# Kernel tuning notes

Hardware: AMD Instinct MI355X
Metric: run time of the kernel (lower is better)

Reference implementation:

```python
import jax, jax.numpy as jnp
import numpy as np

NUM_HEADS = 8
OUT_FEATURES = 64
ALPHA = 0.2


def setup_inputs() -> dict:
    key = jax.random.key(0)
    k1, k2, k3, k4 = jax.random.split(key, 4)
    B, N, E, F_IN = 2, 8192, 4096, 256
    x = jax.random.normal(k1, (B, N, F_IN), dtype=jnp.float32)
    H = jax.random.uniform(k2, (N, E), dtype=jnp.float32)
    # xavier-like scaled params
    W = jax.random.normal(k3, (F_IN, OUT_FEATURES * NUM_HEADS), dtype=jnp.float32) * 0.05
    a_vertices = jax.random.normal(k4, (OUT_FEATURES, 1), dtype=jnp.float32) * 0.1
    return {"x": x, "H": H, "W": W, "a_vertices": a_vertices}


def reference(x, H, W, a_vertices):
    B, N, _ = x.shape
    # Wh: (B, N, heads, out)
    Wh = jnp.matmul(x, W).reshape(B, N, NUM_HEADS, OUT_FEATURES)
    # per-node, per-head attention logit: (B, N, heads)
    av = jax.nn.leaky_relu(jnp.einsum('bnhd,d->bnh', Wh, a_vertices[:, 0]), ALPHA)
    # edge attention: softmax over edges (torch dim=0 of (E, heads))
    ae = jax.nn.softmax(jnp.einsum('ne,bnh->beh', H, av), axis=1)  # (B, E, heads)
    # aggregate node features onto edges: (B, E, heads, out)
    m = jnp.einsum('ne,bnhd->behd', H, Wh)
    # scatter back to nodes with edge-attention weighting: (B, N, heads, out)
    out = jnp.einsum('ne,beh,behd->bnhd', H, ae, m)
    return out.reshape(B, N, NUM_HEADS * OUT_FEATURES)
```

## Files before the change

### kernel.cpp

```cpp
#include <hip/hip_runtime.h>

#define N_NODES 8192
#define N_EDGES 4096
#define F_INS   256
#define HEADS   8
#define DOUT    64
#define HDIM    512
#define CCOMB   1024
#define BATCH   2

typedef __bf16 bf16x8 __attribute__((ext_vector_type(8)));
typedef __bf16 bf16x4 __attribute__((ext_vector_type(4)));
typedef float  f32x4  __attribute__((ext_vector_type(4)));

__device__ __forceinline__ void gld_lds16(const __bf16* g, __bf16* l) {
    __builtin_amdgcn_global_load_lds(
        (const __attribute__((address_space(1))) void*)g,
        (__attribute__((address_space(3))) void*)l, 16, 0, 0);
}

__launch_bounds__(256)
__global__ void convert_H_logits_kernel(const float* __restrict__ H,
                                        const float* __restrict__ av,
                                        __bf16* __restrict__ Hb,
                                        __bf16* __restrict__ HbT,
                                        float* __restrict__ logits) {
    __shared__ float lav[512 * 16];
    __shared__ __bf16 tile[32][33];
    __shared__ float red[256 * 16];
    int t = threadIdx.x;
    int e0 = blockIdx.x * 32;
    int n0 = blockIdx.y * 512;
    for (int p = t; p < 8192; p += 256) {
        int b = p >> 12, rem = p & 4095, i = rem >> 3, h = rem & 7;
        lav[i * 16 + b * 8 + h] = av[(size_t)b * (N_NODES * 8) + (size_t)(n0 + i) * 8 + h];
    }
    __syncthreads();
    int c = t & 31, r0 = t >> 5;
    float acc[16];
#pragma unroll
    for (int q = 0; q < 16; ++q) acc[q] = 0.f;
    for (int sub = 0; sub < 16; ++sub) {
        int nb = n0 + sub * 32;
#pragma unroll
        for (int p = 0; p < 4; ++p) {
            int r = p * 8 + r0;
            float v = H[(size_t)(nb + r) * N_EDGES + e0 + c];
            __bf16 bv = (__bf16)v;
            Hb[(size_t)(nb + r) * N_EDGES + e0 + c] = bv;
            tile[r][c] = bv;
            const float* lr = &lav[(sub * 32 + r) * 16];
#pragma unroll
            for (int q = 0; q < 16; ++q) acc[q] += v * lr[q];
        }
        __syncthreads();
#pragma unroll
        for (int p = 0; p < 4; ++p) {
            int er = p * 8 + r0;
            HbT[(size_t)(e0 + er) * N_NODES + nb + c] = tile[c][er];
        }
        __syncthreads();
    }
#pragma unroll
    for (int q = 0; q < 16; ++q) red[t * 16 + q] = acc[q];
    __syncthreads();
    for (int o = t; o < 512; o += 256) {
        int e = o & 31, q = o >> 5;
        float s = 0.f;
#pragma unroll
        for (int r8 = 0; r8 < 8; ++r8) s += red[(r8 * 32 + e) * 16 + q];
        atomicAdd(&logits[(size_t)q * N_EDGES + e0 + e], s);
    }
}

__launch_bounds__(256)
__global__ void wbt_kernel(const float* __restrict__ W, __bf16* __restrict__ WbT) {
    int i = blockIdx.x * 256 + threadIdx.x;
    int c = i >> 8, f = i & 255;
    WbT[i] = (__bf16)W[(size_t)f * HDIM + c];
}

__launch_bounds__(256)
__global__ void wa_kernel(const float* __restrict__ W, const float* __restrict__ a,
                          float* __restrict__ Wa) {
    int i = blockIdx.x * 256 + threadIdx.x;
    if (i >= F_INS * HEADS) return;
    int f = i >> 3, h = i & 7;
    float s = 0.f;
#pragma unroll 8
    for (int d = 0; d < DOUT; ++d) s += W[(size_t)f * HDIM + h * DOUT + d] * a[d];
    Wa[i] = s;
}

__launch_bounds__(256)
__global__ void av_kernel(const float* __restrict__ x, const float* __restrict__ Wa,
                          float* __restrict__ av, __bf16* __restrict__ xb) {
    __shared__ float lx[32][257];
    __shared__ float lwa[F_INS * HEADS];
    int t = threadIdx.x;
    size_t row0 = (size_t)blockIdx.x * 32;
    for (int p = t; p < F_INS * HEADS; p += 256) lwa[p] = Wa[p];
#pragma unroll
    for (int p = 0; p < 32; ++p) {
        float v = x[(row0 + p) * F_INS + t];
        lx[p][t] = v;
        xb[(row0 + p) * F_INS + t] = (__bf16)v;
    }
    __syncthreads();
    int r = t >> 3, h = t & 7;
    float acc = 0.f;
#pragma unroll 8
    for (int f = 0; f < F_INS; ++f) acc += lx[r][f] * lwa[f * 8 + h];
    av[(row0 + r) * 8 + h] = acc > 0.f ? acc : 0.2f * acc;
}

__launch_bounds__(256)
__global__ void softmax_kernel(float* __restrict__ logits) {
    __shared__ float red[4];
    __shared__ float reds[4];
    int t = threadIdx.x;
    float* row = logits + (size_t)blockIdx.x * N_EDGES;
    float mx = -1e30f;
    for (int i = t; i < N_EDGES; i += 256) mx = fmaxf(mx, row[i]);
#pragma unroll
    for (int o = 32; o > 0; o >>= 1) mx = fmaxf(mx, __shfl_xor(mx, o, 64));
    if ((t & 63) == 0) red[t >> 6] = mx;
    __syncthreads();
    mx = fmaxf(fmaxf(red[0], red[1]), fmaxf(red[2], red[3]));
    float s = 0.f;
    for (int i = t; i < N_EDGES; i += 256) {
        float v = expf(row[i] - mx);
        row[i] = v;
        s += v;
    }
#pragma unroll
    for (int o = 32; o > 0; o >>= 1) s += __shfl_xor(s, o, 64);
    if ((t & 63) == 0) reds[t >> 6] = s;
    __syncthreads();
    float inv = 1.0f / (reds[0] + reds[1] + reds[2] + reds[3]);
    for (int i = t; i < N_EDGES; i += 256) row[i] *= inv;
}

template <int MODE>
__launch_bounds__(256, 4)
__global__ void gemm_bt(const __bf16* __restrict__ A, const __bf16* __restrict__ BT,
                        int lda, int ldbt, int K,
                        size_t a_bz, size_t bt_bz, size_t out_z,
                        __bf16* __restrict__ outB, int ldo,
                        float* __restrict__ outF) {
    __shared__ __bf16 AsF[8192];
    __shared__ __bf16 BsF[8192];
    int t = threadIdx.x;
    int bz = blockIdx.z;
    A  += (size_t)bz * a_bz;
    BT += (size_t)bz * bt_bz;
    if (MODE == 0) outB += (size_t)bz * out_z;
    if (MODE == 1) outF += (size_t)bz * out_z;
    size_t m0 = (size_t)blockIdx.y * 128;
    size_t n0 = (size_t)blockIdx.x * 128;

    int lane = t & 63, wv = t >> 6;
    int ln = lane & 15, lk = lane >> 4;

    const __bf16* pA[4]; const __bf16* pB[4];
    __bf16* lA[4]; __bf16* lB[4];
#pragma unroll
    for (int p = 0; p < 4; ++p) {
        int bid = wv * 4 + p;
        int mb = bid >> 1, kb = bid & 1;
        pA[p] = A + (m0 + mb * 16 + ln) * (size_t)lda + kb * 32 + lk * 8;
        pB[p] = BT + (n0 + mb * 16 + ln) * (size_t)ldbt + kb * 32 + lk * 8;
        lA[p] = &AsF[bid * 512];
        lB[p] = &BsF[bid * 512];
    }

    int wm16 = (wv & 1) * 4, wn16 = (wv >> 1) * 4;
    f32x4 acc[4][4] = {};

    for (int k0 = 0; k0 < K; k0 += 64) {
        __syncthreads();
#pragma unroll
        for (int p = 0; p < 4; ++p) gld_lds16(pA[p] + k0, lA[p]);
#pragma unroll
        for (int p = 0; p < 4; ++p) gld_lds16(pB[p] + k0, lB[p]);
        __syncthreads();
#pragma unroll
        for (int ksb = 0; ksb < 2; ++ksb) {
            bf16x8 af[4], bfr[4];
#pragma unroll
            for (int i = 0; i < 4; ++i)
                af[i] = *(const bf16x8*)&AsF[((wm16 + i) * 2 + ksb) * 512 + lane * 8];
#pragma unroll
            for (int j = 0; j < 4; ++j)
                bfr[j] = *(const bf16x8*)&BsF[((wn16 + j) * 2 + ksb) * 512 + lane * 8];
#pragma unroll
            for (int i = 0; i < 4; ++i)
#pragma unroll
                for (int j = 0; j < 4; ++j)
                    acc[i][j] = __builtin_amdgcn_mfma_f32_16x16x32_bf16(
                        af[i], bfr[j], acc[i][j], 0, 0, 0);
        }
    }

    int wm = (wv & 1) * 64, wn = (wv >> 1) * 64;
#pragma unroll
    for (int i = 0; i < 4; ++i)
#pragma unroll
        for (int j = 0; j < 4; ++j)
#pragma unroll
            for (int rg = 0; rg < 4; ++rg) {
                int gm = (int)m0 + wm + i * 16 + lk * 4 + rg;
                int gc = (int)n0 + wn + j * 16 + ln;
                float v = acc[i][j][rg];
                if (MODE == 0) {
                    outB[(size_t)gm * ldo + gc] = (__bf16)v;
                } else if (MODE == 1) {
                    outF[(size_t)gm * ldo + gc] = v;
                } else {
                    outF[(size_t)(gc >> 9) * ((size_t)N_NODES * HDIM) +
                         (size_t)gm * HDIM + (gc & 511)] = v;
                }
            }
}

template <int SWZ>
__launch_bounds__(512, 2)
__global__ void gemm256(const __bf16* __restrict__ A, const __bf16* __restrict__ BT,
                        int lda, int ldbt, int K,
                        size_t a_bz, size_t bt_bz, size_t out_z,
                        float* __restrict__ outF, int ldo) {
    __shared__ __bf16 lds[4 * 32 * 512];
    int bx, by, bz;
    if (SWZ) {
        int g = (int)blockIdx.x + 4 * ((int)blockIdx.y + 32 * (int)blockIdx.z);
        int xcd = g & 7, j = g >> 3;
        int l = (j & 3) + 4 * xcd + 32 * (j >> 2);
        bx = l & 3; by = (l >> 2) & 31; bz = l >> 7;
    } else {
        bx = blockIdx.x; by = blockIdx.y; bz = blockIdx.z;
    }
    A    += (size_t)bz * a_bz;
    BT   += (size_t)bz * bt_bz;
    outF += (size_t)bz * out_z;
    size_t m0 = (size_t)by * 256;
    size_t n0 = (size_t)bx * 256;

    int t = threadIdx.x;
    int lane = t & 63, wv = t >> 6;
    int ln = lane & 15, lk = lane >> 4;

    int fw = wv * 2;
    const __bf16* gA0 = A + (m0 + fw * 16 + ln) * (size_t)lda + lk * 8;
    const __bf16* gA1 = gA0 + 16 * (size_t)lda;
    const __bf16* gB0 = BT + (n0 + fw * 16 + ln) * (size_t)ldbt + lk * 8;
    const __bf16* gB1 = gB0 + 16 * (size_t)ldbt;

    int NT = K >> 5;

    for (int tt = 0; tt < 3; ++tt) {
        __bf16* d = &lds[tt * 16384];
        gld_lds16(gA0 + tt * 32, d + fw * 512);
        gld_lds16(gA1 + tt * 32, d + (fw + 1) * 512);
        gld_lds16(gB0 + tt * 32, d + (16 + fw) * 512);
        gld_lds16(gB1 + tt * 32, d + (16 + fw + 1) * 512);
    }
    asm volatile("s_waitcnt vmcnt(8)" ::: "memory");
    __builtin_amdgcn_s_barrier();
    __builtin_amdgcn_sched_barrier(0);

    f32x4 acc[8][4] = {};
    int wmf = (wv >> 2) * 8;
    int wnf = (wv & 3) * 4;

    auto compute = [&](int tl) {
        const __bf16* buf = &lds[(tl & 3) * 16384];
        bf16x8 af[8], bfr[4];
#pragma unroll
        for (int i = 0; i < 8; ++i)
            af[i] = *(const bf16x8*)(buf + (wmf + i) * 512 + lane * 8);
#pragma unroll
        for (int j = 0; j < 4; ++j)
            bfr[j] = *(const bf16x8*)(buf + (16 + wnf + j) * 512 + lane * 8);
        __builtin_amdgcn_s_setprio(1);
#pragma unroll
        for (int i = 0; i < 8; ++i)
#pragma unroll
            for (int j = 0; j < 4; ++j)
                acc[i][j] = __builtin_amdgcn_mfma_f32_16x16x32_bf16(
                    af[i], bfr[j], acc[i][j], 0, 0, 0);
        __builtin_amdgcn_s_setprio(0);
    };

    for (int tl = 0; tl < NT - 3; ++tl) {
        __bf16* d = &lds[((tl + 3) & 3) * 16384];
        int off = (tl + 3) * 32;
        gld_lds16(gA0 + off, d + fw * 512);
        gld_lds16(gA1 + off, d + (fw + 1) * 512);
        gld_lds16(gB0 + off, d + (16 + fw) * 512);
        gld_lds16(gB1 + off, d + (16 + fw + 1) * 512);
        compute(tl);
        asm volatile("s_waitcnt vmcnt(8)" ::: "memory");
        __builtin_amdgcn_s_barrier();
        __builtin_amdgcn_sched_barrier(0);
    }
    compute(NT - 3);
    asm volatile("s_waitcnt vmcnt(4)" ::: "memory");
    __builtin_amdgcn_s_barrier();
    __builtin_amdgcn_sched_barrier(0);
    compute(NT - 2);
    asm volatile("s_waitcnt vmcnt(0)" ::: "memory");
    __builtin_amdgcn_s_barrier();
    __builtin_amdgcn_sched_barrier(0);
    compute(NT - 1);

    int wm = (wv >> 2) * 128, wn = (wv & 3) * 64;
#pragma unroll
    for (int i = 0; i < 8; ++i)
#pragma unroll
        for (int j = 0; j < 4; ++j)
#pragma unroll
            for (int rg = 0; rg < 4; ++rg) {
                int gm = (int)m0 + wm + i * 16 + lk * 4 + rg;
                int gc = (int)n0 + wn + j * 16 + ln;
                outF[(size_t)gm * ldo + gc] = acc[i][j][rg];
            }
}

__launch_bounds__(256)
__global__ void scale1_kernel(const float* __restrict__ acc1, const float* __restrict__ ae,
                              __bf16* __restrict__ mwT) {
    int i = blockIdx.x * 256 + threadIdx.x;
    size_t base = (size_t)i * 4;
    int c = (int)(base >> 12);
    int e = (int)(base & 4095);
    const size_t slab = (size_t)CCOMB * N_EDGES / 4;
    float4 s0 = ((const float4*)acc1)[i];
    float4 s1 = ((const float4*)acc1)[i + slab];
    float4 s2 = ((const float4*)acc1)[i + 2 * slab];
    float4 s3 = ((const float4*)acc1)[i + 3 * slab];
    float4 a4 = *(const float4*)(ae + ((size_t)(c >> 6) << 12) + e);
    bf16x4 o;
    o.x = (__bf16)((s0.x + s1.x + s2.x + s3.x) * a4.x);
    o.y = (__bf16)((s0.y + s1.y + s2.y + s3.y) * a4.y);
    o.z = (__bf16)((s0.z + s1.z + s2.z + s3.z) * a4.z);
    o.w = (__bf16)((s0.w + s1.w + s2.w + s3.w) * a4.w);
    ((bf16x4*)mwT)[i] = o;
}

__launch_bounds__(256)
__global__ void reduce2_kernel(const float* __restrict__ s, float* __restrict__ out) {
    int i = blockIdx.x * 256 + threadIdx.x;
    size_t base = (size_t)i * 4;
    int m = (int)(base >> 10);
    int c = (int)(base & 1023);
    const size_t slab = (size_t)N_NODES * CCOMB / 4;
    float4 a = ((const float4*)s)[i];
    float4 b = ((const float4*)s)[i + slab];
    float4 o;
    o.x = a.x + b.x; o.y = a.y + b.y; o.z = a.z + b.z; o.w = a.w + b.w;
    *(float4*)&out[(size_t)(c >> 9) * ((size_t)N_NODES * HDIM) +
                   (size_t)m * HDIM + (c & 511)] = o;
}

extern "C" void kernel_launch(void* const* d_in, const int* in_sizes, int n_in,
                              void* d_out, int out_size, void* d_ws, size_t ws_size,
                              hipStream_t stream) {
    const float* x = (const float*)d_in[0];
    const float* H = (const float*)d_in[1];
    const float* W = (const float*)d_in[2];
    const float* a = (const float*)d_in[3];
    float* out = (float*)d_out;

    char* p = (char*)d_ws;
    __bf16* Hb   = (__bf16*)p; p += (size_t)N_NODES * N_EDGES * 2;
    __bf16* HbT  = (__bf16*)p; p += (size_t)N_EDGES * N_NODES * 2;
    __bf16* xb   = (__bf16*)p; p += (size_t)BATCH * N_NODES * F_INS * 2;
    __bf16* WbT  = (__bf16*)p; p += (size_t)HDIM * F_INS * 2;
    __bf16* WhbT = (__bf16*)p; p += (size_t)CCOMB * N_NODES * 2;
    __bf16* mwT  = (__bf16*)p; p += (size_t)CCOMB * N_EDGES * 2;
    float*  Wa   = (float*)p;  p += (size_t)F_INS * HEADS * 4;
    float*  av   = (float*)p;  p += (size_t)BATCH * N_NODES * HEADS * 4;
    float*  ae   = (float*)p;  p += (size_t)16 * N_EDGES * 4;
    float*  acc1 = (float*)p;  p += (size_t)4 * CCOMB * N_EDGES * 4;

    hipMemsetAsync(ae, 0, (size_t)16 * N_EDGES * 4, stream);

    wbt_kernel<<<dim3(HDIM * F_INS / 256), 256, 0, stream>>>(W, WbT);
    wa_kernel<<<dim3(8), 256, 0, stream>>>(W, a, Wa);
    av_kernel<<<dim3(BATCH * N_NODES / 32), 256, 0, stream>>>(x, Wa, av, xb);
    convert_H_logits_kernel<<<dim3(N_EDGES / 32, N_NODES / 512), 256, 0, stream>>>(
        H, av, Hb, HbT, ae);
    softmax_kernel<<<dim3(16), 256, 0, stream>>>(ae);

    gemm_bt<0><<<dim3(64, 4, 2), 256, 0, stream>>>(
        WbT, xb, F_INS, F_INS, F_INS,
        0, (size_t)N_NODES * F_INS, (size_t)HDIM * N_NODES,
        WhbT, N_NODES, nullptr);

    gemm256<0><<<dim3(16, 4, 4), 512, 0, stream>>>(
        WhbT, HbT, N_NODES, N_NODES, 2048,
        2048, 2048, (size_t)CCOMB * N_EDGES,
        acc1, N_EDGES);

    scale1_kernel<<<dim3(CCOMB * N_EDGES / 4 / 256), 256, 0, stream>>>(acc1, ae, mwT);

    gemm256<1><<<dim3(4, 32, 2), 512, 0, stream>>>(
        Hb, mwT, N_EDGES, N_EDGES, 2048,
        2048, 2048, (size_t)N_NODES * CCOMB,
        acc1, CCOMB);

    reduce2_kernel<<<dim3(N_NODES * CCOMB / 4 / 256), 256, 0, stream>>>(acc1, out);
}
```

Before: 485.7 us.

## Vectorize H conversion kernel and replace atomic logits with two-stage reduction

Rewrites the H-to-bf16 conversion and logits kernel to use wider tiles (128 edges by 256 nodes), float4 loads, bf16x4/bf16x8 stores, and a double-buffered transpose tile so HbT writes overlap the next group's loads. The atomicAdd accumulation of logits is replaced by per-block partial sums written to scratch (reusing acc1) and a separate reduce kernel, which also removes the memset. This targets the bandwidth-bound conversion pass that reads 128MB of fp32 H and writes two bf16 copies. In exchange it adds a kernel launch and more register pressure from the 64-float accumulator.

```diff
diff --git a/kernel.cpp b/kernel.cpp
--- a/kernel.cpp
+++ b/kernel.cpp
@@ -19,58 +19,130 @@
         (__attribute__((address_space(3))) void*)l, 16, 0, 0);
 }
 
-__launch_bounds__(256)
+__launch_bounds__(256, 4)
 __global__ void convert_H_logits_kernel(const float* __restrict__ H,
                                         const float* __restrict__ av,
                                         __bf16* __restrict__ Hb,
                                         __bf16* __restrict__ HbT,
-                                        float* __restrict__ logits) {
-    __shared__ float lav[512 * 16];
-    __shared__ __bf16 tile[32][33];
-    __shared__ float red[256 * 16];
+                                        float* __restrict__ plog) {
+    __shared__ __align__(16) char smem[33280];
+    float* lav = (float*)smem;
+    __bf16 (*tile)[32][132] = (__bf16(*)[32][132])(smem + 16384);
+    float* red = (float*)smem;
+
     int t = threadIdx.x;
-    int e0 = blockIdx.x * 32;
-    int n0 = blockIdx.y * 512;
-    for (int p = t; p < 8192; p += 256) {
-        int b = p >> 12, rem = p & 4095, i = rem >> 3, h = rem & 7;
-        lav[i * 16 + b * 8 + h] = av[(size_t)b * (N_NODES * 8) + (size_t)(n0 + i) * 8 + h];
-    }
-    __syncthreads();
-    int c = t & 31, r0 = t >> 5;
-    float acc[16];
-#pragma unroll
-    for (int q = 0; q < 16; ++q) acc[q] = 0.f;
-    for (int sub = 0; sub < 16; ++sub) {
-        int nb = n0 + sub * 32;
-#pragma unroll
-        for (int p = 0; p < 4; ++p) {
-            int r = p * 8 + r0;
-            float v = H[(size_t)(nb + r) * N_EDGES + e0 + c];
-            __bf16 bv = (__bf16)v;
-            Hb[(size_t)(nb + r) * N_EDGES + e0 + c] = bv;
-            tile[r][c] = bv;
-            const float* lr = &lav[(sub * 32 + r) * 16];
-#pragma unroll
-            for (int q = 0; q < 16; ++q) acc[q] += v * lr[q];
+    int e0 = blockIdx.x * 128;
+    int n0 = blockIdx.y * 256;
+    int equad = t & 31, r0 = t >> 5;
+    int lane = t & 63, wv = t >> 6;
+
+    for (int p = t; p < 4096; p += 256) {
+        int n = p >> 4, q = p & 15, b = q >> 3, h = q & 7;
+        lav[p] = av[(size_t)b * (N_NODES * 8) + (size_t)(n0 + n) * 8 + h];
+    }
+
+    const float* hbase = H + (size_t)n0 * N_EDGES + e0 + equad * 4;
+    __bf16* hb_base = Hb + (size_t)n0 * N_EDGES + e0 + equad * 4;
+
+    f32x4 acc[4][4] = {};
+
+    __syncthreads();
+
+    float4 v[4];
+    for (int g = 0; g < 8; ++g) {
+        int nb = g * 32;
+#pragma unroll
+        for (int k = 0; k < 4; ++k) {
+            int n = nb + r0 + 8 * k;
+            v[k] = *(const float4*)(hbase + (size_t)n * N_EDGES);
+        }
+        if (g > 0) {
+            int pb = (g - 1) & 1, pnb = (g - 1) * 32;
+#pragma unroll
+            for (int s = 0; s < 2; ++s) {
+                int id = s * 256 + t;
+                int er = id >> 2, oct = id & 3;
+                bf16x8 val;
+#pragma unroll
+                for (int j = 0; j < 8; ++j) val[j] = tile[pb][oct * 8 + j][er];
+                *(bf16x8*)(HbT + (size_t)(e0 + er) * N_NODES + n0 + pnb + oct * 8) = val;
+            }
+        }
+        int buf = g & 1;
+#pragma unroll
+        for (int k = 0; k < 4; ++k) {
+            int n = nb + r0 + 8 * k;
+            const f32x4* lrow = (const f32x4*)&lav[n * 16];
+            float4 vv = v[k];
+#pragma unroll
+            for (int qq = 0; qq < 4; ++qq) {
+                f32x4 l = lrow[qq];
+                acc[0][qq] += l * vv.x;
+                acc[1][qq] += l * vv.y;
+                acc[2][qq] += l * vv.z;
+                acc[3][qq] += l * vv.w;
+            }
+            bf16x4 hb;
+            hb.x = (__bf16)vv.x; hb.y = (__bf16)vv.y;
+            hb.z = (__bf16)vv.z; hb.w = (__bf16)vv.w;
+            *(bf16x4*)(hb_base + (size_t)n * N_EDGES) = hb;
+            *(bf16x4*)&tile[buf][r0 + 8 * k][equad * 4] = hb;
         }
         __syncthreads();
-#pragma unroll
-        for (int p = 0; p < 4; ++p) {
-            int er = p * 8 + r0;
-            HbT[(size_t)(e0 + er) * N_NODES + nb + c] = tile[c][er];
+    }
+    {
+        int pnb = 7 * 32;
+#pragma unroll
+        for (int s = 0; s < 2; ++s) {
+            int id = s * 256 + t;
+            int er = id >> 2, oct = id & 3;
+            bf16x8 val;
+#pragma unroll
+            for (int j = 0; j < 8; ++j) val[j] = tile[1][oct * 8 + j][er];
+            *(bf16x8*)(HbT + (size_t)(e0 + er) * N_NODES + n0 + pnb + oct * 8) = val;
         }
-        __syncthreads();
-    }
-#pragma unroll
-    for (int q = 0; q < 16; ++q) red[t * 16 + q] = acc[q];
-    __syncthreads();
-    for (int o = t; o < 512; o += 256) {
-        int e = o & 31, q = o >> 5;
-        float s = 0.f;
-#pragma unroll
-        for (int r8 = 0; r8 < 8; ++r8) s += red[(r8 * 32 + e) * 16 + q];
-        atomicAdd(&logits[(size_t)q * N_EDGES + e0 + e], s);
-    }
+    }
+
+#pragma unroll
+    for (int ec = 0; ec < 4; ++ec)
+#pragma unroll
+        for (int qq = 0; qq < 4; ++qq)
+#pragma unroll
+            for (int qi = 0; qi < 4; ++qi)
+                acc[ec][qq][qi] += __shfl_xor(acc[ec][qq][qi], 32, 64);
+
+    __syncthreads();
+    if (lane < 32) {
+#pragma unroll
+        for (int qq = 0; qq < 4; ++qq)
+#pragma unroll
+            for (int qi = 0; qi < 4; ++qi) {
+                f32x4 tmp = {acc[0][qq][qi], acc[1][qq][qi],
+                             acc[2][qq][qi], acc[3][qq][qi]};
+                *(f32x4*)&red[wv * 2048 + (qq * 4 + qi) * 128 + equad * 4] = tmp;
+            }
+    }
+    __syncthreads();
+#pragma unroll
+    for (int s = 0; s < 8; ++s) {
+        int id = s * 256 + t;
+        int q = id >> 7, el = id & 127;
+        float sum = red[q * 128 + el] + red[2048 + q * 128 + el] +
+                    red[4096 + q * 128 + el] + red[6144 + q * 128 + el];
+        plog[((size_t)blockIdx.y * 16 + q) * N_EDGES + e0 + el] = sum;
+    }
+}
+
+__launch_bounds__(256)
+__global__ void reduce_logits_kernel(const float* __restrict__ plog,
+                                     float* __restrict__ logits) {
+    int id = blockIdx.x * 256 + threadIdx.x;
+    int q = id >> 12, e = id & 4095;
+    float s = 0.f;
+#pragma unroll
+    for (int nb = 0; nb < 32; ++nb)
+        s += plog[((size_t)nb * 16 + q) * N_EDGES + e];
+    logits[(size_t)q * N_EDGES + e] = s;
 }
 
 __launch_bounds__(256)
@@ -382,14 +454,14 @@
     float*  av   = (float*)p;  p += (size_t)BATCH * N_NODES * HEADS * 4;
     float*  ae   = (float*)p;  p += (size_t)16 * N_EDGES * 4;
     float*  acc1 = (float*)p;  p += (size_t)4 * CCOMB * N_EDGES * 4;
-
-    hipMemsetAsync(ae, 0, (size_t)16 * N_EDGES * 4, stream);
+    float*  plog = acc1;
 
     wbt_kernel<<<dim3(HDIM * F_INS / 256), 256, 0, stream>>>(W, WbT);
     wa_kernel<<<dim3(8), 256, 0, stream>>>(W, a, Wa);
     av_kernel<<<dim3(BATCH * N_NODES / 32), 256, 0, stream>>>(x, Wa, av, xb);
-    convert_H_logits_kernel<<<dim3(N_EDGES / 32, N_NODES / 512), 256, 0, stream>>>(
-        H, av, Hb, HbT, ae);
+    convert_H_logits_kernel<<<dim3(N_EDGES / 128, N_NODES / 256), 256, 0, stream>>>(
+        H, av, Hb, HbT, plog);
+    reduce_logits_kernel<<<dim3(256), 256, 0, stream>>>(plog, ae);
     softmax_kernel<<<dim3(16), 256, 0, stream>>>(ae);
 
     gemm_bt<0><<<dim3(64, 4, 2), 256, 0, stream>>>(
```

Result: no change. 485.3 us (-0.1%).
